# Optimization experiments

Measured on AMD Instinct MI355X. Metric: run time of the kernel, lower is better.

Reference implementation:

```python
import jax, jax.numpy as jnp
import numpy as np

N = 100000      # nodes
E = 1600000     # edges
F_IN = 512      # input features
H = 64          # hidden
R = 2           # relations
B = 30          # bases
NEG_SLOPE = 0.2 # GATConv default


def setup_inputs() -> dict:
    key = jax.random.key(0)
    ks = jax.random.split(key, 14)
    s_in = 1.0 / np.sqrt(F_IN)
    s_h = 1.0 / np.sqrt(H)
    return {
        "x": jax.random.normal(ks[0], (N, F_IN), jnp.float32),
        "edge_index": jax.random.randint(ks[1], (2, E), 0, N),
        "edge_types": jax.random.randint(ks[2], (E,), 0, R),
        # RGCN layer 1 (F_IN -> H), basis-decomposed
        "basis1": jax.random.normal(ks[3], (B, F_IN, H), jnp.float32) * s_in,
        "comp1": jax.random.normal(ks[4], (R, B), jnp.float32) * (1.0 / np.sqrt(B)),
        "root1": jax.random.normal(ks[5], (F_IN, H), jnp.float32) * s_in,
        "bias1": jnp.zeros((H,), jnp.float32),
        # RGCN layer 2 (H -> H)
        "basis2": jax.random.normal(ks[6], (B, H, H), jnp.float32) * s_h,
        "comp2": jax.random.normal(ks[7], (R, B), jnp.float32) * (1.0 / np.sqrt(B)),
        "root2": jax.random.normal(ks[8], (H, H), jnp.float32) * s_h,
        "bias2": jnp.zeros((H,), jnp.float32),
        # GAT (H -> 1, heads=1)
        "gat_w": jax.random.normal(ks[9], (H, 1), jnp.float32) * s_h,
        "att_src": jax.random.normal(ks[10], (1,), jnp.float32),
        "att_dst": jax.random.normal(ks[11], (1,), jnp.float32),
        "gat_bias": jnp.zeros((1,), jnp.float32),
    }


def rgcn_layer(x, src, dst, etype, basis, comp, root, bias):
    # W_r = sum_b comp[r,b] * basis[b]; transform nodes once per relation,
    # then gather per edge (math-equal to PyG's per-edge transform, cheaper).
    W = jnp.einsum('rb,bio->rio', comp, basis)       # [R, in, out]
    h = jnp.einsum('ni,rio->rno', x, W)              # [R, N, out]
    out = x @ root + bias                            # root/self term
    for r in range(R):                               # R=2, fixed small loop
        m = (etype == r).astype(x.dtype)             # [E]
        msg = h[r][src] * m[:, None]                 # gather + mask
        agg = jax.ops.segment_sum(msg, dst, num_segments=N)
        cnt = jax.ops.segment_sum(m, dst, num_segments=N)
        out = out + agg / jnp.maximum(cnt, 1.0)[:, None]   # mean aggr per relation
    return out


def gat_layer(x, src, dst, gat_w, att_src, att_dst, gat_bias):
    # GATConv with heads=1, out=1, add_self_loops=True, negative_slope=0.2
    loop = jnp.arange(N)
    s = jnp.concatenate([src, loop])
    d = jnp.concatenate([dst, loop])
    h = x @ gat_w                                    # [N, 1]
    a_s = h[:, 0] * att_src[0]                       # [N]
    a_d = h[:, 0] * att_dst[0]                       # [N]
    e = jax.nn.leaky_relu(a_s[s] + a_d[d], NEG_SLOPE)  # [E+N]
    emax = jax.ops.segment_max(e, d, num_segments=N)   # every dst has self-loop
    ex = jnp.exp(e - emax[d])
    denom = jax.ops.segment_sum(ex, d, num_segments=N)
    alpha = ex / denom[d]                            # segment softmax over dst
    out = jax.ops.segment_sum(alpha[:, None] * h[s], d, num_segments=N)
    return out + gat_bias


def reference(x, edge_index, edge_types,
              basis1, comp1, root1, bias1,
              basis2, comp2, root2, bias2,
              gat_w, att_src, att_dst, gat_bias):
    src, dst = edge_index[0], edge_index[1]
    x1 = jax.nn.relu(rgcn_layer(x, src, dst, edge_types, basis1, comp1, root1, bias1))
    x2 = rgcn_layer(x1, src, dst, edge_types, basis2, comp2, root2, bias2)
    return gat_layer(x2, src, dst, gat_w, att_src, att_dst, gat_bias)  # [N, 1]
```

## Files before the change

### kernel.cpp

```cpp
#include <hip/hip_runtime.h>
#include <hip/hip_bf16.h>
#include <math.h>

#define NCOL 192
#define BB   30
#define SCAN_T 256
#define SCAN_ELEMS 1024

typedef short bf16x8 __attribute__((ext_vector_type(8)));
typedef float f32x4  __attribute__((ext_vector_type(4)));
typedef unsigned short u16x8 __attribute__((ext_vector_type(8)));

__device__ __forceinline__ ushort f2bf(float f) {
  unsigned u = __float_as_uint(f);
  unsigned r = u + 0x7fff + ((u >> 16) & 1);
  return (ushort)(r >> 16);
}
__device__ __forceinline__ float bf2f(ushort u) {
  return __uint_as_float(((unsigned)u) << 16);
}

__global__ void zero_int(int* __restrict__ p, int n) {
  int i = blockIdx.x * blockDim.x + threadIdx.x;
  if (i < n) p[i] = 0;
}

__global__ void hist_deg(const int* __restrict__ dst, int* __restrict__ deg, int E) {
  int e = blockIdx.x * blockDim.x + threadIdx.x;
  if (e >= E) return;
  atomicAdd(&deg[dst[e]], 1);
}

__global__ __launch_bounds__(SCAN_T) void scan_local(const int* __restrict__ deg,
                                                     int* __restrict__ rowptr,
                                                     int* __restrict__ partial, int N) {
  __shared__ int sdata[SCAN_T];
  int t = threadIdx.x;
  int base = blockIdx.x * SCAN_ELEMS + t * 4;
  int v[4], s = 0;
#pragma unroll
  for (int k = 0; k < 4; ++k) {
    v[k] = (base + k < N) ? deg[base + k] : 0;
    s += v[k];
  }
  sdata[t] = s;
  __syncthreads();
  for (int off = 1; off < SCAN_T; off <<= 1) {
    int add = (t >= off) ? sdata[t - off] : 0;
    __syncthreads();
    sdata[t] += add;
    __syncthreads();
  }
  int run = sdata[t] - s;
  if (t == SCAN_T - 1) partial[blockIdx.x] = sdata[t];
#pragma unroll
  for (int k = 0; k < 4; ++k) {
    if (base + k < N) rowptr[base + k] = run;
    run += v[k];
  }
}

__global__ __launch_bounds__(SCAN_T) void scan_partial(int* __restrict__ partial, int nb) {
  __shared__ int sdata[SCAN_T];
  int t = threadIdx.x;
  int v = (t < nb) ? partial[t] : 0;
  sdata[t] = v;
  __syncthreads();
  for (int off = 1; off < SCAN_T; off <<= 1) {
    int add = (t >= off) ? sdata[t - off] : 0;
    __syncthreads();
    sdata[t] += add;
    __syncthreads();
  }
  if (t < nb) partial[t] = sdata[t] - v;
  if (t == nb - 1) partial[nb] = sdata[t];
}

__global__ void scan_add(int* __restrict__ rowptr, const int* __restrict__ partial,
                         int* __restrict__ fill, int N) {
  int i = blockIdx.x * blockDim.x + threadIdx.x;
  if (i < N) {
    rowptr[i] += partial[i / SCAN_ELEMS];
    fill[i] = 0;
  }
  if (i == N) rowptr[N] = partial[(N + SCAN_ELEMS - 1) / SCAN_ELEMS];
}

__global__ void scatter_edges(const int* __restrict__ src, const int* __restrict__ dst,
                              const int* __restrict__ et, const int* __restrict__ rowptr,
                              int* __restrict__ fill, int* __restrict__ srcpk, int E) {
  int e = blockIdx.x * blockDim.x + threadIdx.x;
  if (e >= E) return;
  int d = dst[e];
  int pos = rowptr[d] + atomicAdd(&fill[d], 1);
  srcpk[pos] = src[e] | (et[e] << 30);
}

__global__ void build_wpk(const float* __restrict__ basis, const float* __restrict__ comp,
                          const float* __restrict__ root, ushort* __restrict__ Wpk, int Kin) {
  int idx = blockIdx.x * blockDim.x + threadIdx.x;
  if (idx >= Kin * NCOL) return;
  int k = idx / NCOL, j = idx - k * NCOL;
  float v;
  if (j < 64) {
    v = root[k * 64 + j];
  } else {
    int r = (j >> 6) - 1, o = j & 63;
    float s = 0.f;
#pragma unroll
    for (int b = 0; b < BB; ++b)
      s = fmaf(comp[r * BB + b], basis[((size_t)b * Kin + k) * 64 + o], s);
    v = s;
  }
  Wpk[(((size_t)(k >> 3) * NCOL + j) << 3) + (k & 7)] = f2bf(v);
}

template <int K, int BF16IN>
__global__ __launch_bounds__(256, 4) void gemm_mfma(const void* __restrict__ Xv,
                                                    const ushort* __restrict__ Wpk,
                                                    ushort* __restrict__ Y, int N) {
  constexpr int BK  = 64;
  constexpr int NC  = K / BK;
  constexpr int NLD = BF16IN ? (64 * (BK / 8) / 256) : (64 * (BK / 4) / 256);
  __shared__ ushort As[(NC > 1 ? 2 : 1) * 64 * BK];

  const int row0 = blockIdx.x * 64;
  const int tid  = threadIdx.x;
  const int wid  = tid >> 6;
  const int lane = tid & 63;
  const int lrow = lane & 15;
  const int lhi  = lane >> 4;

  const float*  Xf = (const float*)Xv;
  const ushort* Xh = (const ushort*)Xv;

  float4 pf[BF16IN ? 1 : NLD];
  u16x8  pfh[BF16IN ? NLD : 1];

#define LOAD_CHUNK(c)                                                              \
  if constexpr (BF16IN) {                                                          \
    _Pragma("unroll") for (int it = 0; it < NLD; ++it) {                           \
      int idx = tid + it * 256;                                                    \
      int row = idx / (BK / 8), kq = idx - row * (BK / 8);                         \
      int r = row0 + row;                                                          \
      pfh[it] = (u16x8){0, 0, 0, 0, 0, 0, 0, 0};                                   \
      if (r < N) pfh[it] = ((const u16x8*)Xh)[(size_t)r * (K / 8) + (c) * (BK / 8) + kq]; \
    }                                                                              \
  } else {                                                                         \
    _Pragma("unroll") for (int it = 0; it < NLD; ++it) {                           \
      int idx = tid + it * 256;                                                    \
      int row = idx / (BK / 4), kq = idx - row * (BK / 4);                         \
      int r = row0 + row;                                                          \
      pf[it] = make_float4(0.f, 0.f, 0.f, 0.f);                                    \
      if (r < N) pf[it] = ((const float4*)Xf)[(size_t)r * (K / 4) + (c) * (BK / 4) + kq]; \
    }                                                                              \
  }

#define COMMIT_CHUNK(buf)                                                          \
  {                                                                                \
    char* Aw = (char*)As + (size_t)(buf) * 64 * BK * 2;                            \
    if constexpr (BF16IN) {                                                        \
      _Pragma("unroll") for (int it = 0; it < NLD; ++it) {                         \
        int idx = tid + it * 256;                                                  \
        int row = idx / (BK / 8), kq = idx - row * (BK / 8);                       \
        int byte = ((row * BK + kq * 8) * 2) ^ ((row & 7) << 4);                   \
        *(u16x8*)(Aw + byte) = pfh[it];                                            \
      }                                                                            \
    } else {                                                                       \
      _Pragma("unroll") for (int it = 0; it < NLD; ++it) {                         \
        int idx = tid + it * 256;                                                  \
        int row = idx / (BK / 4), kq = idx - row * (BK / 4);                       \
        ushort4 b;                                                                 \
        b.x = f2bf(pf[it].x); b.y = f2bf(pf[it].y);                                \
        b.z = f2bf(pf[it].z); b.w = f2bf(pf[it].w);                                \
        int byte = ((row * BK + kq * 4) * 2) ^ ((row & 7) << 4);                   \
        *(ushort4*)(Aw + byte) = b;                                                \
      }                                                                            \
    }                                                                              \
  }

  LOAD_CHUNK(0)
  COMMIT_CHUNK(0)
  __syncthreads();

  f32x4 acc[4][3];
#pragma unroll
  for (int s = 0; s < 4; ++s)
#pragma unroll
    for (int c = 0; c < 3; ++c) acc[s][c] = (f32x4){0.f, 0.f, 0.f, 0.f};

  for (int c = 0; c < NC; ++c) {
    if (c + 1 < NC) { LOAD_CHUNK(c + 1) }
    const char* Ab = (const char*)As + (size_t)(NC > 1 ? (c & 1) : 0) * 64 * BK * 2;
#pragma unroll
    for (int t = 0; t < BK / 32; ++t) {
      int g = (c * (BK / 32) + t) * 4 + lhi;
      const bf16x8* bp = (const bf16x8*)Wpk + (size_t)g * NCOL + wid * 48 + lrow;
      bf16x8 b0 = bp[0];
      bf16x8 b1 = bp[16];
      bf16x8 b2 = bp[32];
      bf16x8 a[4];
#pragma unroll
      for (int s = 0; s < 4; ++s) {
        int arow = s * 16 + lrow;
        int abyte = ((arow * BK + t * 32 + lhi * 8) * 2) ^ ((arow & 7) << 4);
        a[s] = *(const bf16x8*)(Ab + abyte);
      }
#pragma unroll
      for (int s = 0; s < 4; ++s) {
        acc[s][0] = __builtin_amdgcn_mfma_f32_16x16x32_bf16(a[s], b0, acc[s][0], 0, 0, 0);
        acc[s][1] = __builtin_amdgcn_mfma_f32_16x16x32_bf16(a[s], b1, acc[s][1], 0, 0, 0);
        acc[s][2] = __builtin_amdgcn_mfma_f32_16x16x32_bf16(a[s], b2, acc[s][2], 0, 0, 0);
      }
    }
    if (c + 1 < NC) {
      __syncthreads();
      COMMIT_CHUNK((c + 1) & 1)
      __syncthreads();
    }
  }
#undef LOAD_CHUNK
#undef COMMIT_CHUNK

#pragma unroll
  for (int s = 0; s < 4; ++s) {
#pragma unroll
    for (int cc = 0; cc < 3; ++cc) {
#pragma unroll
      for (int j = 0; j < 4; ++j) {
        int r = row0 + s * 16 + lhi * 4 + j;
        if (r < N) Y[(size_t)r * NCOL + wid * 48 + cc * 16 + lrow] = f2bf(acc[s][cc][j]);
      }
    }
  }
}

template <int RELU, int GATH>
__global__ __launch_bounds__(256) void fused_agg(const ushort* __restrict__ Y,
                                                 const int* __restrict__ rowptr,
                                                 const int* __restrict__ srcpk,
                                                 const float* __restrict__ bias,
                                                 const float* __restrict__ gw,
                                                 ushort* __restrict__ accout,
                                                 float* __restrict__ hval, int N) {
  int n = blockIdx.x * 4 + (threadIdx.x >> 6);
  if (n >= N) return;
  int lane = threadIdx.x & 63;
  float a0 = 0.f, a1 = 0.f;
  int c0 = 0, c1 = 0;
  int beg = rowptr[n], end = rowptr[n + 1];
  int i = beg;
  for (; i + 3 < end; i += 4) {
    int pk[4];
    float v[4];
#pragma unroll
    for (int u = 0; u < 4; ++u) pk[u] = srcpk[i + u];
#pragma unroll
    for (int u = 0; u < 4; ++u) {
      int s = pk[u] & 0x3fffffff, r = pk[u] >> 30;
      v[u] = bf2f(Y[(size_t)s * NCOL + 64 + (r << 6) + lane]);
    }
#pragma unroll
    for (int u = 0; u < 4; ++u) {
      if (pk[u] >> 30) { a1 += v[u]; c1++; } else { a0 += v[u]; c0++; }
    }
  }
  for (; i < end; ++i) {
    int pk = srcpk[i];
    int s = pk & 0x3fffffff, r = pk >> 30;
    float v = bf2f(Y[(size_t)s * NCOL + 64 + (r << 6) + lane]);
    if (r) { a1 += v; c1++; } else { a0 += v; c0++; }
  }
  float res = bf2f(Y[(size_t)n * NCOL + lane]) + bias[lane]
            + a0 / (float)(c0 > 1 ? c0 : 1) + a1 / (float)(c1 > 1 ? c1 : 1);
  if (RELU) res = fmaxf(res, 0.f);
  if (accout) accout[(size_t)n * 64 + lane] = f2bf(res);
  if (GATH) {
    float v = res * gw[lane];
#pragma unroll
    for (int o = 32; o > 0; o >>= 1) v += __shfl_down(v, o);
    if (lane == 0) hval[n] = v;
  }
}

__device__ __forceinline__ float leaky(float x) { return x > 0.f ? x : 0.2f * x; }

__global__ __launch_bounds__(256) void gat_csr(const int* __restrict__ rowptr,
                                               const int* __restrict__ srcpk,
                                               const float* __restrict__ hval,
                                               const float* __restrict__ as_,
                                               const float* __restrict__ ad_,
                                               const float* __restrict__ gb,
                                               float* __restrict__ out, int N) {
  int n = blockIdx.x * blockDim.x + threadIdx.x;
  if (n >= N) return;
  float as = *as_, ad = *ad_;
  float hv = hval[n];
  float adn = hv * ad;
  float eself = leaky(hv * as + adn);
  float m = eself;
  int beg = rowptr[n], end = rowptr[n + 1];
  for (int i = beg; i < end; ++i) {
    int s = srcpk[i] & 0x3fffffff;
    float e = leaky(hval[s] * as + adn);
    m = fmaxf(m, e);
  }
  float den = expf(eself - m);
  float acc = den * hv;
  for (int i = beg; i < end; ++i) {
    int s = srcpk[i] & 0x3fffffff;
    float hs = hval[s];
    float e = leaky(hs * as + adn);
    float ex = expf(e - m);
    den += ex;
    acc += ex * hs;
  }
  out[n] = acc / den + *gb;
}

extern "C" void kernel_launch(void* const* d_in, const int* in_sizes, int n_in,
                              void* d_out, int out_size, void* d_ws, size_t ws_size,
                              hipStream_t stream) {
  const float* x      = (const float*)d_in[0];
  const int*   eidx   = (const int*)d_in[1];
  const int*   etype  = (const int*)d_in[2];
  const float* basis1 = (const float*)d_in[3];
  const float* comp1  = (const float*)d_in[4];
  const float* root1  = (const float*)d_in[5];
  const float* bias1  = (const float*)d_in[6];
  const float* basis2 = (const float*)d_in[7];
  const float* comp2  = (const float*)d_in[8];
  const float* root2  = (const float*)d_in[9];
  const float* bias2  = (const float*)d_in[10];
  const float* gat_w  = (const float*)d_in[11];
  const float* att_s  = (const float*)d_in[12];
  const float* att_d  = (const float*)d_in[13];
  const float* gat_b  = (const float*)d_in[14];

  const int N = in_sizes[0] / 512;
  const int E = in_sizes[1] / 2;
  const int* src = eidx;
  const int* dst = eidx + E;

  char* p = (char*)d_ws;
  ushort* Y    = (ushort*)p; p += (size_t)N * NCOL * 2;
  ushort* acc1 = (ushort*)p; p += (size_t)N * 64 * 2;
  ushort* Wpk  = (ushort*)p; p += (size_t)512 * NCOL * 2;
  float* hval  = (float*)p;  p += (size_t)N * 4;
  int* deg     = (int*)p;    p += (size_t)N * 4;
  int* rowptr  = (int*)p;    p += (size_t)(N + 16) * 4;
  int* partial = (int*)p;    p += (size_t)(SCAN_T + 16) * 4;
  int* srcpk   = (int*)p;    p += (size_t)E * 4;
  float* out   = (float*)d_out;
  int* fill    = deg;

  const int TB = 256;
  const int GB = (N + 63) / 64;
  const int nb = (N + SCAN_ELEMS - 1) / SCAN_ELEMS;

  zero_int<<<(N + TB - 1) / TB, TB, 0, stream>>>(deg, N);
  hist_deg<<<(E + TB - 1) / TB, TB, 0, stream>>>(dst, deg, E);
  scan_local<<<nb, SCAN_T, 0, stream>>>(deg, rowptr, partial, N);
  scan_partial<<<1, SCAN_T, 0, stream>>>(partial, nb);
  scan_add<<<(N + 1 + TB - 1) / TB, TB, 0, stream>>>(rowptr, partial, fill, N);
  scatter_edges<<<(E + TB - 1) / TB, TB, 0, stream>>>(src, dst, etype, rowptr, fill, srcpk, E);

  build_wpk<<<(512 * NCOL + TB - 1) / TB, TB, 0, stream>>>(basis1, comp1, root1, Wpk, 512);
  gemm_mfma<512, 0><<<GB, 256, 0, stream>>>(x, Wpk, Y, N);
  fused_agg<1, 0><<<(N + 3) / 4, TB, 0, stream>>>(Y, rowptr, srcpk, bias1, nullptr, acc1,
                                                  nullptr, N);

  build_wpk<<<(64 * NCOL + TB - 1) / TB, TB, 0, stream>>>(basis2, comp2, root2, Wpk, 64);
  gemm_mfma<64, 1><<<GB, 256, 0, stream>>>(acc1, Wpk, Y, N);
  fused_agg<0, 1><<<(N + 3) / 4, TB, 0, stream>>>(Y, rowptr, srcpk, bias2, gat_w, nullptr,
                                                  hval, N);

  gat_csr<<<(N + TB - 1) / TB, TB, 0, stream>>>(rowptr, srcpk, hval, att_s, att_d, gat_b,
                                                out, N);
}
```

Baseline: 431.4 us.

## Vectorize neighbor gather in aggregation and parallelize GAT softmax per wave

The RGCN aggregation kernel now has each lane load 8 bf16 features at once, with 8 edge groups per wave processing 16 edges per iteration. Partial sums and per-relation counts are then reduced across groups with xor shuffles. The GAT kernel changes from one thread per node to one 64-lane wave per node, computing the segment max and softmax sums with shuffles, plus a fast path for degree up to 64. The aim is more memory-level parallelism and less serial per-thread edge looping, at the cost of more shuffle reductions and idle lanes for low-degree nodes.

```diff
diff --git a/kernel.cpp b/kernel.cpp
--- a/kernel.cpp
+++ b/kernel.cpp
@@ -245,41 +245,81 @@
                                                  float* __restrict__ hval, int N) {
   int n = blockIdx.x * 4 + (threadIdx.x >> 6);
   if (n >= N) return;
-  int lane = threadIdx.x & 63;
-  float a0 = 0.f, a1 = 0.f;
-  int c0 = 0, c1 = 0;
-  int beg = rowptr[n], end = rowptr[n + 1];
-  int i = beg;
-  for (; i + 3 < end; i += 4) {
-    int pk[4];
-    float v[4];
-#pragma unroll
-    for (int u = 0; u < 4; ++u) pk[u] = srcpk[i + u];
-#pragma unroll
-    for (int u = 0; u < 4; ++u) {
-      int s = pk[u] & 0x3fffffff, r = pk[u] >> 30;
-      v[u] = bf2f(Y[(size_t)s * NCOL + 64 + (r << 6) + lane]);
-    }
-#pragma unroll
-    for (int u = 0; u < 4; ++u) {
-      if (pk[u] >> 30) { a1 += v[u]; c1++; } else { a0 += v[u]; c0++; }
-    }
-  }
-  for (; i < end; ++i) {
-    int pk = srcpk[i];
-    int s = pk & 0x3fffffff, r = pk >> 30;
-    float v = bf2f(Y[(size_t)s * NCOL + 64 + (r << 6) + lane]);
-    if (r) { a1 += v; c1++; } else { a0 += v; c0++; }
-  }
-  float res = bf2f(Y[(size_t)n * NCOL + lane]) + bias[lane]
-            + a0 / (float)(c0 > 1 ? c0 : 1) + a1 / (float)(c1 > 1 ? c1 : 1);
-  if (RELU) res = fmaxf(res, 0.f);
-  if (accout) accout[(size_t)n * 64 + lane] = f2bf(res);
+  const int lane = threadIdx.x & 63;
+  const int g    = lane >> 3;
+  const int f0   = (lane & 7) * 8;
+
+  float a0[8], a1[8];
+#pragma unroll
+  for (int j = 0; j < 8; ++j) { a0[j] = 0.f; a1[j] = 0.f; }
+  float c0 = 0.f, c1 = 0.f;
+
+  const int beg = rowptr[n], end = rowptr[n + 1];
+  for (int i = beg; i < end; i += 16) {
+    int eA = i + g, eB = i + 8 + g;
+    bool vA = eA < end, vB = eB < end;
+    int pkA = 0, pkB = 0;
+    if (vA) pkA = srcpk[eA];
+    if (vB) pkB = srcpk[eB];
+    u16x8 xA = (u16x8){0, 0, 0, 0, 0, 0, 0, 0}, xB = xA;
+    if (vA) xA = *(const u16x8*)(Y + (size_t)(pkA & 0x3fffffff) * NCOL + 64 +
+                                 ((pkA >> 30) << 6) + f0);
+    if (vB) xB = *(const u16x8*)(Y + (size_t)(pkB & 0x3fffffff) * NCOL + 64 +
+                                 ((pkB >> 30) << 6) + f0);
+    float rA = (vA && (pkA >> 30)) ? 1.f : 0.f;
+    float sA = vA ? 1.f : 0.f;
+    float rB = (vB && (pkB >> 30)) ? 1.f : 0.f;
+    float sB = vB ? 1.f : 0.f;
+    c0 += (sA - rA) + (sB - rB);
+    c1 += rA + rB;
+#pragma unroll
+    for (int j = 0; j < 8; ++j) {
+      float fA = bf2f(xA[j]), fB = bf2f(xB[j]);
+      a0[j] += (sA - rA) * fA + (sB - rB) * fB;
+      a1[j] += rA * fA + rB * fB;
+    }
+  }
+
+#pragma unroll
+  for (int msk = 8; msk <= 32; msk <<= 1) {
+#pragma unroll
+    for (int j = 0; j < 8; ++j) {
+      a0[j] += __shfl_xor(a0[j], msk);
+      a1[j] += __shfl_xor(a1[j], msk);
+    }
+    c0 += __shfl_xor(c0, msk);
+    c1 += __shfl_xor(c1, msk);
+  }
+
+  float inv0 = 1.f / fmaxf(c0, 1.f);
+  float inv1 = 1.f / fmaxf(c1, 1.f);
+  u16x8 rv = *(const u16x8*)(Y + (size_t)n * NCOL + f0);
+  float4 bA = *(const float4*)(bias + f0);
+  float4 bB = *(const float4*)(bias + f0 + 4);
+  float bb[8] = {bA.x, bA.y, bA.z, bA.w, bB.x, bB.y, bB.z, bB.w};
+  float res[8];
+#pragma unroll
+  for (int j = 0; j < 8; ++j) {
+    float v = bf2f(rv[j]) + bb[j] + a0[j] * inv0 + a1[j] * inv1;
+    res[j] = RELU ? fmaxf(v, 0.f) : v;
+  }
+  if (accout && g == 0) {
+    u16x8 o;
+#pragma unroll
+    for (int j = 0; j < 8; ++j) o[j] = f2bf(res[j]);
+    *(u16x8*)(accout + (size_t)n * 64 + f0) = o;
+  }
   if (GATH) {
-    float v = res * gw[lane];
-#pragma unroll
-    for (int o = 32; o > 0; o >>= 1) v += __shfl_down(v, o);
-    if (lane == 0) hval[n] = v;
+    float4 gA = *(const float4*)(gw + f0);
+    float4 gB = *(const float4*)(gw + f0 + 4);
+    float gg[8] = {gA.x, gA.y, gA.z, gA.w, gB.x, gB.y, gB.z, gB.w};
+    float dot = 0.f;
+#pragma unroll
+    for (int j = 0; j < 8; ++j) dot = fmaf(res[j], gg[j], dot);
+    dot += __shfl_xor(dot, 1);
+    dot += __shfl_xor(dot, 2);
+    dot += __shfl_xor(dot, 4);
+    if (lane == 0) hval[n] = dot;
   }
 }
 
@@ -292,30 +332,57 @@
                                                const float* __restrict__ ad_,
                                                const float* __restrict__ gb,
                                                float* __restrict__ out, int N) {
-  int n = blockIdx.x * blockDim.x + threadIdx.x;
+  int n = blockIdx.x * 4 + (threadIdx.x >> 6);
   if (n >= N) return;
+  const int lane = threadIdx.x & 63;
   float as = *as_, ad = *ad_;
   float hv = hval[n];
   float adn = hv * ad;
   float eself = leaky(hv * as + adn);
-  float m = eself;
   int beg = rowptr[n], end = rowptr[n + 1];
-  for (int i = beg; i < end; ++i) {
-    int s = srcpk[i] & 0x3fffffff;
-    float e = leaky(hval[s] * as + adn);
-    m = fmaxf(m, e);
-  }
-  float den = expf(eself - m);
-  float acc = den * hv;
-  for (int i = beg; i < end; ++i) {
-    int s = srcpk[i] & 0x3fffffff;
-    float hs = hval[s];
-    float e = leaky(hs * as + adn);
-    float ex = expf(e - m);
-    den += ex;
-    acc += ex * hs;
-  }
-  out[n] = acc / den + *gb;
+  int deg = end - beg;
+  float m, den, acc;
+  if (deg <= 64) {
+    bool valid = lane < deg;
+    float hs = 0.f;
+    if (valid) hs = hval[srcpk[beg + lane] & 0x3fffffff];
+    float e = valid ? leaky(hs * as + adn) : -3.4e38f;
+    m = fmaxf(e, eself);
+#pragma unroll
+    for (int o = 32; o > 0; o >>= 1) m = fmaxf(m, __shfl_xor(m, o));
+    float ex = valid ? expf(e - m) : 0.f;
+    den = ex;
+    acc = ex * hs;
+#pragma unroll
+    for (int o = 32; o > 0; o >>= 1) {
+      den += __shfl_xor(den, o);
+      acc += __shfl_xor(acc, o);
+    }
+  } else {
+    m = eself;
+    for (int i = beg + lane; i < end; i += 64)
+      m = fmaxf(m, leaky(hval[srcpk[i] & 0x3fffffff] * as + adn));
+#pragma unroll
+    for (int o = 32; o > 0; o >>= 1) m = fmaxf(m, __shfl_xor(m, o));
+    float dl = 0.f, al = 0.f;
+    for (int i = beg + lane; i < end; i += 64) {
+      float hs = hval[srcpk[i] & 0x3fffffff];
+      float ex = expf(leaky(hs * as + adn) - m);
+      dl += ex;
+      al += ex * hs;
+    }
+    den = dl;
+    acc = al;
+#pragma unroll
+    for (int o = 32; o > 0; o >>= 1) {
+      den += __shfl_xor(den, o);
+      acc += __shfl_xor(acc, o);
+    }
+  }
+  float es = expf(eself - m);
+  den += es;
+  acc += es * hv;
+  if (lane == 0) out[n] = acc / den + *gb;
 }
 
 extern "C" void kernel_launch(void* const* d_in, const int* in_sizes, int n_in,
@@ -375,6 +442,6 @@
   fused_agg<0, 1><<<(N + 3) / 4, TB, 0, stream>>>(Y, rowptr, srcpk, bias2, gat_w, nullptr,
                                                   hval, N);
 
-  gat_csr<<<(N + TB - 1) / TB, TB, 0, stream>>>(rowptr, srcpk, hval, att_s, att_d, gat_b,
-                                                out, N);
-}
+  gat_csr<<<(N + 3) / 4, TB, 0, stream>>>(rowptr, srcpk, hval, att_s, att_d, gat_b,
+                                          out, N);
+}
```

After: 410.7 us. -4.8%, faster.
